# Performance work log

Hardware: AMD Instinct MI355X
Metric: run time of the kernel (lower is better)

Reference implementation:

```python
import jax, jax.numpy as jnp
import numpy as np

NUM_NODES = 100000
OUT_CHANNELS = 32
NUM_EDGES = 3200000


def setup_inputs() -> dict:
    key = jax.random.key(0)
    k1, k2, k3 = jax.random.split(key, 3)
    edge_index = jax.random.randint(k1, (2, NUM_EDGES), 0, NUM_NODES, dtype=jnp.int64)
    # nn.Linear init: weight [out, in], uniform(-1/sqrt(in), 1/sqrt(in))
    bound = 1.0 / np.sqrt(NUM_NODES)
    W = jax.random.uniform(k2, (OUT_CHANNELS, NUM_NODES), jnp.float32, -bound, bound)
    b = jax.random.uniform(k3, (OUT_CHANNELS,), jnp.float32, -bound, bound)
    return {"edge_index": edge_index, "W": W, "b": b}


def reference(edge_index, W, b):
    # LINK forward: A = sparse COO [N, num_nodes] with 1.0 per edge (duplicates sum),
    # logits = A @ W.T + b. Implemented as gather + segment_sum (no dense A).
    row = edge_index[0]
    col = edge_index[1]
    row = row - row.min()  # faithful to `row = row - row.min()`
    gathered = jnp.take(W.T, col, axis=0)  # [E, out_channels]
    logits = jax.ops.segment_sum(gathered, row, num_segments=NUM_NODES)  # [N, out]
    return logits + b
```

## Files before the change

kernel.cpp:

```cpp
#include <hip/hip_runtime.h>

#define NUM_NODES 100000
#define OUT_CH 32
#define NUM_EDGES 3200000

#define RPB 128
#define NB 782
#define CAP2 5120
#define TPB_BIN 1024
#define TILE 12800
#define KPT 13
#define NTILE 250
#define TPB 512
#define TR_BLOCKS 3125
#define MIN_BLOCKS 256

static __device__ __forceinline__ unsigned short f32_to_bf16_rne(float f) {
    unsigned u = __float_as_uint(f);
    unsigned r = u + 0x7FFFu + ((u >> 16) & 1u);
    return (unsigned short)(r >> 16);
}
static __device__ __forceinline__ float bf16_to_f32(unsigned short h) {
    return __uint_as_float(((unsigned)h) << 16);
}

__global__ void __launch_bounds__(256)
fused_pre(const float* __restrict__ W, ushort4* __restrict__ Wt,
          const int4* __restrict__ row4, int* __restrict__ partmin,
          int* __restrict__ bcount) {
    int bk = blockIdx.x;
    int t  = threadIdx.x;
    if (bk < TR_BLOCKS) {
        __shared__ float tile[32][33];
        int tx = t & 31, ty = t >> 5;
        int colBase = bk * 32;
        #pragma unroll
        for (int k = 0; k < 4; k++) {
            int c = ty + 8 * k;
            tile[c][tx] = W[c * NUM_NODES + colBase + tx];
        }
        __syncthreads();
        int lc = t >> 3, q = t & 7;
        ushort4 o;
        o.x = f32_to_bf16_rne(tile[q * 4 + 0][lc]);
        o.y = f32_to_bf16_rne(tile[q * 4 + 1][lc]);
        o.z = f32_to_bf16_rne(tile[q * 4 + 2][lc]);
        o.w = f32_to_bf16_rne(tile[q * 4 + 3][lc]);
        Wt[(size_t)(colBase + lc) * 8 + q] = o;
    } else if (bk < TR_BLOCKS + MIN_BLOCKS) {
        int mb  = bk - TR_BLOCKS;
        int tid = mb * 256 + t;
        int m = 0x7fffffff;
        for (int i = tid; i < NUM_EDGES / 4; i += MIN_BLOCKS * 256) {
            int4 v = row4[i];
            m = min(m, min(min(v.x, v.y), min(v.z, v.w)));
        }
        #pragma unroll
        for (int off = 32; off > 0; off >>= 1) m = min(m, __shfl_down(m, off, 64));
        __shared__ int wm[4];
        if ((t & 63) == 0) wm[t >> 6] = m;
        __syncthreads();
        if (t == 0) partmin[mb] = min(min(wm[0], wm[1]), min(wm[2], wm[3]));
    } else {
        for (int i = t; i < NB; i += 256) bcount[i] = 0;
    }
}

__global__ void __launch_bounds__(TPB_BIN)
bin_stage(const int* __restrict__ edge, const int* __restrict__ partmin,
          int* __restrict__ bcount, unsigned int* __restrict__ bin) {
    __shared__ int cnt[NB];
    __shared__ int cur[NB];
    __shared__ int rminS;
    int t = threadIdx.x;
    if (t < 64) {
        int m = min(min(partmin[t], partmin[t + 64]),
                    min(partmin[t + 128], partmin[t + 192]));
        #pragma unroll
        for (int off = 32; off > 0; off >>= 1) m = min(m, __shfl_down(m, off, 64));
        if (t == 0) rminS = m;
    }
    for (int i = t; i < NB; i += TPB_BIN) cnt[i] = 0;
    __syncthreads();
    int rmin = rminS;
    int eb = blockIdx.x * TILE;

    unsigned int ent[KPT];
    int bb[KPT];
    #pragma unroll
    for (int k = 0; k < KPT; k++) {
        int o = k * TPB_BIN + t;
        bb[k] = -1;
        if (o < TILE) {
            int e = eb + o;
            int r = edge[e] - rmin;
            int c = edge[NUM_EDGES + e];
            int b = r >> 7;
            bb[k]  = b;
            ent[k] = ((unsigned int)(r & 127) << 17) | (unsigned int)c;
            atomicAdd(&cnt[b], 1);
        }
    }
    __syncthreads();

    for (int i = t; i < NB; i += TPB_BIN) cur[i] = cnt[i] ? atomicAdd(&bcount[i], cnt[i]) : 0;
    __syncthreads();

    #pragma unroll
    for (int k = 0; k < KPT; k++) {
        if (bb[k] >= 0) {
            int pos = atomicAdd(&cur[bb[k]], 1);
            if (pos < CAP2) bin[(size_t)bb[k] * CAP2 + pos] = ent[k];
        }
    }
}

__global__ void __launch_bounds__(TPB)
bucket_gather(const unsigned int* __restrict__ bin, const int* __restrict__ bcount,
              const ushort4* __restrict__ Wt, const float* __restrict__ b,
              float* __restrict__ out) {
    __shared__ int cnt2[RPB * 8];
    __shared__ int cur2[RPB * 8];
    __shared__ int rowstart[RPB];
    __shared__ int rowcnt[RPB];
    __shared__ int scn[RPB];
    __shared__ int lcol[CAP2];

    int t = threadIdx.x;
    int bk = blockIdx.x;
    int n = bcount[bk];
    if (n > CAP2) n = CAP2;
    const unsigned int* mybin = bin + (size_t)bk * CAP2;

    for (int i = t; i < RPB * 8; i += TPB) cnt2[i] = 0;
    __syncthreads();

    for (int i = t; i < n; i += TPB) {
        unsigned int p = mybin[i];
        int lr  = p >> 17;
        int seg = (p & 0x1FFFF) >> 14;
        atomicAdd(&cnt2[(lr << 3) | seg], 1);
    }
    __syncthreads();

    if (t < RPB) {
        int s = 0;
        #pragma unroll
        for (int k = 0; k < 8; k++) s += cnt2[(t << 3) | k];
        rowcnt[t] = s;
        scn[t] = s;
    }
    __syncthreads();
    for (int off = 1; off < RPB; off <<= 1) {
        int v = (t < RPB && t >= off) ? scn[t - off] : 0;
        __syncthreads();
        if (t < RPB) scn[t] += v;
        __syncthreads();
    }
    if (t < RPB) {
        int rs = scn[t] - rowcnt[t];
        rowstart[t] = rs;
        int run = rs;
        #pragma unroll
        for (int k = 0; k < 8; k++) { cur2[(t << 3) | k] = run; run += cnt2[(t << 3) | k]; }
    }
    __syncthreads();

    for (int i = t; i < n; i += TPB) {
        unsigned int p = mybin[i];
        int lr = p >> 17;
        int c  = p & 0x1FFFF;
        int pos = atomicAdd(&cur2[(lr << 3) | (c >> 14)], 1);
        lcol[pos] = c;
    }
    __syncthreads();

    int g   = t >> 3;
    int sub = t & 7;
    float4 bias = ((const float4*)b)[sub];
    int lrA = g, lrB = g + 64;
    int rowA = bk * RPB + lrA;
    int rowB = bk * RPB + lrB;
    int iA = rowstart[lrA], eA = iA + rowcnt[lrA];
    int iB = rowstart[lrB], eB = iB + rowcnt[lrB];
    bool vA = rowA < NUM_NODES;
    bool vB = rowB < NUM_NODES;
    if (!vA) { iA = eA = 0; }
    if (!vB) { iB = eB = 0; }
    float4 accA = bias, accB = bias;
    int nPair = min(eA - iA, eB - iB);
    for (int k = 0; k < nPair; k++) {
        ushort4 wA = Wt[(size_t)lcol[iA + k] * 8 + sub];
        ushort4 wB = Wt[(size_t)lcol[iB + k] * 8 + sub];
        accA.x += bf16_to_f32(wA.x); accA.y += bf16_to_f32(wA.y);
        accA.z += bf16_to_f32(wA.z); accA.w += bf16_to_f32(wA.w);
        accB.x += bf16_to_f32(wB.x); accB.y += bf16_to_f32(wB.y);
        accB.z += bf16_to_f32(wB.z); accB.w += bf16_to_f32(wB.w);
    }
    iA += nPair; iB += nPair;
    for (; iA < eA; iA++) {
        ushort4 w = Wt[(size_t)lcol[iA] * 8 + sub];
        accA.x += bf16_to_f32(w.x); accA.y += bf16_to_f32(w.y);
        accA.z += bf16_to_f32(w.z); accA.w += bf16_to_f32(w.w);
    }
    for (; iB < eB; iB++) {
        ushort4 w = Wt[(size_t)lcol[iB] * 8 + sub];
        accB.x += bf16_to_f32(w.x); accB.y += bf16_to_f32(w.y);
        accB.z += bf16_to_f32(w.z); accB.w += bf16_to_f32(w.w);
    }
    if (vA) ((float4*)out)[(size_t)rowA * 8 + sub] = accA;
    if (vB) ((float4*)out)[(size_t)rowB * 8 + sub] = accB;
}

extern "C" void kernel_launch(void* const* d_in, const int* in_sizes, int n_in,
                              void* d_out, int out_size, void* d_ws, size_t ws_size,
                              hipStream_t stream) {
    const int*   edge = (const int*)d_in[0];
    const float* W    = (const float*)d_in[1];
    const float* b    = (const float*)d_in[2];
    float* out = (float*)d_out;

    char* ws = (char*)d_ws;
    int*          partmin = (int*)ws;
    int*          bcount  = (int*)(ws + 1024);
    ushort4*      Wt      = (ushort4*)(ws + 8192);
    unsigned int* bin     = (unsigned int*)(ws + 6422528);

    fused_pre<<<TR_BLOCKS + MIN_BLOCKS + 1, 256, 0, stream>>>(W, Wt, (const int4*)edge, partmin, bcount);
    bin_stage<<<NTILE, TPB_BIN, 0, stream>>>(edge, partmin, bcount, bin);
    bucket_gather<<<NB, TPB, 0, stream>>>(bin, bcount, Wt, b, out);
}
```

Measured before the change: 152.2 us.

## Stage binned edges in shared memory to coalesce global bin writes

The binning kernel now scatters each tile's entries into a shared-memory buffer sorted by bucket, using a block-wide prefix scan over bucket counts. Each thread then finds its element's bucket by binary search and writes to global memory, so consecutive threads write consecutive addresses within a bucket instead of scattering randomly. This adds a scan, a second shared-memory pass, a per-element binary search and about 60KB of extra shared memory per block, which may reduce occupancy.

```diff
diff --git a/kernel.cpp b/kernel.cpp
--- a/kernel.cpp
+++ b/kernel.cpp
@@ -69,8 +69,10 @@
 __global__ void __launch_bounds__(TPB_BIN)
 bin_stage(const int* __restrict__ edge, const int* __restrict__ partmin,
           int* __restrict__ bcount, unsigned int* __restrict__ bin) {
-    __shared__ int cnt[NB];
-    __shared__ int cur[NB];
+    __shared__ unsigned int sent[TILE];
+    __shared__ int scnt[NB];
+    __shared__ int send[NB];
+    __shared__ int gfix[NB];
     __shared__ int rminS;
     int t = threadIdx.x;
     if (t < 64) {
@@ -80,7 +82,7 @@
         for (int off = 32; off > 0; off >>= 1) m = min(m, __shfl_down(m, off, 64));
         if (t == 0) rminS = m;
     }
-    for (int i = t; i < NB; i += TPB_BIN) cnt[i] = 0;
+    if (t < NB) scnt[t] = 0;
     __syncthreads();
     int rmin = rminS;
     int eb = blockIdx.x * TILE;
@@ -98,19 +100,49 @@
             int b = r >> 7;
             bb[k]  = b;
             ent[k] = ((unsigned int)(r & 127) << 17) | (unsigned int)c;
-            atomicAdd(&cnt[b], 1);
-        }
-    }
-    __syncthreads();
-
-    for (int i = t; i < NB; i += TPB_BIN) cur[i] = cnt[i] ? atomicAdd(&bcount[i], cnt[i]) : 0;
+            atomicAdd(&scnt[b], 1);
+        }
+    }
+    __syncthreads();
+
+    if (t < NB) send[t] = scnt[t];
+    __syncthreads();
+    for (int off = 1; off < NB; off <<= 1) {
+        int v = 0;
+        if (t < NB && t >= off) v = send[t - off];
+        __syncthreads();
+        if (t < NB) send[t] += v;
+        __syncthreads();
+    }
+    if (t < NB) {
+        int inc = send[t];
+        int c   = scnt[t];
+        int ex  = inc - c;
+        int gb  = c ? atomicAdd(&bcount[t], c) : 0;
+        gfix[t] = t * CAP2 + gb - ex;
+        send[t] = ex;
+    }
     __syncthreads();
 
     #pragma unroll
     for (int k = 0; k < KPT; k++) {
         if (bb[k] >= 0) {
-            int pos = atomicAdd(&cur[bb[k]], 1);
-            if (pos < CAP2) bin[(size_t)bb[k] * CAP2 + pos] = ent[k];
+            int pos = atomicAdd(&send[bb[k]], 1);
+            sent[pos] = ent[k];
+        }
+    }
+    __syncthreads();
+
+    for (int k = 0; k < KPT; k++) {
+        int i = k * TPB_BIN + t;
+        if (i < TILE) {
+            int lo = 0, hi = NB - 1;
+            while (lo < hi) {
+                int mid = (lo + hi) >> 1;
+                if (send[mid] > i) hi = mid; else lo = mid + 1;
+            }
+            int dest = gfix[lo] + i;
+            if (dest < (lo + 1) * CAP2) bin[dest] = sent[i];
         }
     }
 }
```

After: 151.2 us. Within noise of the previous version (-0.7%).

## Fuse row-min reduction into binning kernel and apply offset at output

Applied to the files above, without the earlier changes.

Folds the row-min reduction and the binning pass into the transpose kernel, so the pipeline runs as two kernels plus memsets instead of three kernels. Edges are binned on raw row indices with a global atomicMin for the minimum, and the row shift is applied only when writing the output. Buckets shrink to 64 rows with 256-thread blocks, and the gather loop is unrolled by two for more loads in flight. In exchange it adds two memset launches and a global atomic. Bucket capacity is halved, so skewed row distributions are more likely to overflow.

```diff
diff --git a/kernel.cpp b/kernel.cpp
--- a/kernel.cpp
+++ b/kernel.cpp
@@ -4,16 +4,15 @@
 #define OUT_CH 32
 #define NUM_EDGES 3200000
 
-#define RPB 128
-#define NB 782
-#define CAP2 5120
-#define TPB_BIN 1024
-#define TILE 12800
-#define KPT 13
-#define NTILE 250
-#define TPB 512
+#define RPB 64
+#define NB 1563
+#define NBG 1564
+#define CAP2 2560
 #define TR_BLOCKS 3125
-#define MIN_BLOCKS 256
+#define BIN_TILE 3072
+#define BIN_KPT 12
+#define BIN_BLOCKS 1042
+#define TPB 256
 
 static __device__ __forceinline__ unsigned short f32_to_bf16_rne(float f) {
     unsigned u = __float_as_uint(f);
@@ -25,9 +24,9 @@
 }
 
 __global__ void __launch_bounds__(256)
-fused_pre(const float* __restrict__ W, ushort4* __restrict__ Wt,
-          const int4* __restrict__ row4, int* __restrict__ partmin,
-          int* __restrict__ bcount) {
+fused_main(const float* __restrict__ W, ushort4* __restrict__ Wt,
+           const int* __restrict__ edge, int* __restrict__ rminG,
+           int* __restrict__ bcount, unsigned int* __restrict__ bin) {
     int bk = blockIdx.x;
     int t  = threadIdx.x;
     if (bk < TR_BLOCKS) {
@@ -47,76 +46,53 @@
         o.z = f32_to_bf16_rne(tile[q * 4 + 2][lc]);
         o.w = f32_to_bf16_rne(tile[q * 4 + 3][lc]);
         Wt[(size_t)(colBase + lc) * 8 + q] = o;
-    } else if (bk < TR_BLOCKS + MIN_BLOCKS) {
-        int mb  = bk - TR_BLOCKS;
-        int tid = mb * 256 + t;
-        int m = 0x7fffffff;
-        for (int i = tid; i < NUM_EDGES / 4; i += MIN_BLOCKS * 256) {
-            int4 v = row4[i];
-            m = min(m, min(min(v.x, v.y), min(v.z, v.w)));
+    } else {
+        int mb = bk - TR_BLOCKS;
+        __shared__ int cnt[NB];
+        __shared__ int cur[NB];
+        __shared__ int wm[4];
+        for (int i = t; i < NB; i += 256) cnt[i] = 0;
+        int base = mb * BIN_TILE;
+        int nval = NUM_EDGES - base; if (nval > BIN_TILE) nval = BIN_TILE;
+        unsigned int ent[BIN_KPT];
+        int bb[BIN_KPT];
+        int rm = 0x7fffffff;
+        __syncthreads();
+        #pragma unroll
+        for (int k = 0; k < BIN_KPT; k++) {
+            int o = k * 256 + t;
+            bb[k] = -1;
+            if (o < nval) {
+                int e = base + o;
+                int r = edge[e];
+                int c = edge[NUM_EDGES + e];
+                rm = min(rm, r);
+                int b = r >> 6;
+                bb[k]  = b;
+                ent[k] = ((unsigned int)(r & 63) << 17) | (unsigned int)c;
+                atomicAdd(&cnt[b], 1);
+            }
         }
         #pragma unroll
-        for (int off = 32; off > 0; off >>= 1) m = min(m, __shfl_down(m, off, 64));
-        __shared__ int wm[4];
-        if ((t & 63) == 0) wm[t >> 6] = m;
-        __syncthreads();
-        if (t == 0) partmin[mb] = min(min(wm[0], wm[1]), min(wm[2], wm[3]));
-    } else {
-        for (int i = t; i < NB; i += 256) bcount[i] = 0;
-    }
-}
-
-__global__ void __launch_bounds__(TPB_BIN)
-bin_stage(const int* __restrict__ edge, const int* __restrict__ partmin,
-          int* __restrict__ bcount, unsigned int* __restrict__ bin) {
-    __shared__ int cnt[NB];
-    __shared__ int cur[NB];
-    __shared__ int rminS;
-    int t = threadIdx.x;
-    if (t < 64) {
-        int m = min(min(partmin[t], partmin[t + 64]),
-                    min(partmin[t + 128], partmin[t + 192]));
-        #pragma unroll
-        for (int off = 32; off > 0; off >>= 1) m = min(m, __shfl_down(m, off, 64));
-        if (t == 0) rminS = m;
-    }
-    for (int i = t; i < NB; i += TPB_BIN) cnt[i] = 0;
-    __syncthreads();
-    int rmin = rminS;
-    int eb = blockIdx.x * TILE;
-
-    unsigned int ent[KPT];
-    int bb[KPT];
-    #pragma unroll
-    for (int k = 0; k < KPT; k++) {
-        int o = k * TPB_BIN + t;
-        bb[k] = -1;
-        if (o < TILE) {
-            int e = eb + o;
-            int r = edge[e] - rmin;
-            int c = edge[NUM_EDGES + e];
-            int b = r >> 7;
-            bb[k]  = b;
-            ent[k] = ((unsigned int)(r & 127) << 17) | (unsigned int)c;
-            atomicAdd(&cnt[b], 1);
-        }
-    }
-    __syncthreads();
-
-    for (int i = t; i < NB; i += TPB_BIN) cur[i] = cnt[i] ? atomicAdd(&bcount[i], cnt[i]) : 0;
-    __syncthreads();
-
-    #pragma unroll
-    for (int k = 0; k < KPT; k++) {
-        if (bb[k] >= 0) {
-            int pos = atomicAdd(&cur[bb[k]], 1);
-            if (pos < CAP2) bin[(size_t)bb[k] * CAP2 + pos] = ent[k];
+        for (int off = 32; off > 0; off >>= 1) rm = min(rm, __shfl_down(rm, off, 64));
+        if ((t & 63) == 0) wm[t >> 6] = rm;
+        __syncthreads();
+        if (t == 0) atomicMin(rminG, min(min(wm[0], wm[1]), min(wm[2], wm[3])));
+        for (int i = t; i < NB; i += 256) cur[i] = cnt[i] ? atomicAdd(&bcount[i], cnt[i]) : 0;
+        __syncthreads();
+        #pragma unroll
+        for (int k = 0; k < BIN_KPT; k++) {
+            if (bb[k] >= 0) {
+                int pos = atomicAdd(&cur[bb[k]], 1);
+                if (pos < CAP2) bin[(size_t)bb[k] * CAP2 + pos] = ent[k];
+            }
         }
     }
 }
 
 __global__ void __launch_bounds__(TPB)
 bucket_gather(const unsigned int* __restrict__ bin, const int* __restrict__ bcount,
+              const int* __restrict__ rminG,
               const ushort4* __restrict__ Wt, const float* __restrict__ b,
               float* __restrict__ out) {
     __shared__ int cnt2[RPB * 8];
@@ -125,10 +101,12 @@
     __shared__ int rowcnt[RPB];
     __shared__ int scn[RPB];
     __shared__ int lcol[CAP2];
+    __shared__ int rminS;
 
     int t = threadIdx.x;
     int bk = blockIdx.x;
-    int n = bcount[bk];
+    if (t == 0) rminS = rminG[0];
+    int n = (bk < NB) ? bcount[bk] : 0;
     if (n > CAP2) n = CAP2;
     const unsigned int* mybin = bin + (size_t)bk * CAP2;
 
@@ -178,18 +156,36 @@
     int g   = t >> 3;
     int sub = t & 7;
     float4 bias = ((const float4*)b)[sub];
-    int lrA = g, lrB = g + 64;
-    int rowA = bk * RPB + lrA;
-    int rowB = bk * RPB + lrB;
+    int rmin = rminS;
+    int lrA = g, lrB = g + 32;
+    int outA = bk * RPB + lrA - rmin;
+    int outB = bk * RPB + lrB - rmin;
+    bool vA = (unsigned)outA < NUM_NODES;
+    bool vB = (unsigned)outB < NUM_NODES;
     int iA = rowstart[lrA], eA = iA + rowcnt[lrA];
     int iB = rowstart[lrB], eB = iB + rowcnt[lrB];
-    bool vA = rowA < NUM_NODES;
-    bool vB = rowB < NUM_NODES;
     if (!vA) { iA = eA = 0; }
     if (!vB) { iB = eB = 0; }
     float4 accA = bias, accB = bias;
     int nPair = min(eA - iA, eB - iB);
-    for (int k = 0; k < nPair; k++) {
+    int k = 0;
+    for (; k + 2 <= nPair; k += 2) {
+        int cA0 = lcol[iA + k],     cB0 = lcol[iB + k];
+        int cA1 = lcol[iA + k + 1], cB1 = lcol[iB + k + 1];
+        ushort4 wA0 = Wt[(size_t)cA0 * 8 + sub];
+        ushort4 wB0 = Wt[(size_t)cB0 * 8 + sub];
+        ushort4 wA1 = Wt[(size_t)cA1 * 8 + sub];
+        ushort4 wB1 = Wt[(size_t)cB1 * 8 + sub];
+        accA.x += bf16_to_f32(wA0.x) + bf16_to_f32(wA1.x);
+        accA.y += bf16_to_f32(wA0.y) + bf16_to_f32(wA1.y);
+        accA.z += bf16_to_f32(wA0.z) + bf16_to_f32(wA1.z);
+        accA.w += bf16_to_f32(wA0.w) + bf16_to_f32(wA1.w);
+        accB.x += bf16_to_f32(wB0.x) + bf16_to_f32(wB1.x);
+        accB.y += bf16_to_f32(wB0.y) + bf16_to_f32(wB1.y);
+        accB.z += bf16_to_f32(wB0.z) + bf16_to_f32(wB1.z);
+        accB.w += bf16_to_f32(wB0.w) + bf16_to_f32(wB1.w);
+    }
+    for (; k < nPair; k++) {
         ushort4 wA = Wt[(size_t)lcol[iA + k] * 8 + sub];
         ushort4 wB = Wt[(size_t)lcol[iB + k] * 8 + sub];
         accA.x += bf16_to_f32(wA.x); accA.y += bf16_to_f32(wA.y);
@@ -208,8 +204,8 @@
         accB.x += bf16_to_f32(w.x); accB.y += bf16_to_f32(w.y);
         accB.z += bf16_to_f32(w.z); accB.w += bf16_to_f32(w.w);
     }
-    if (vA) ((float4*)out)[(size_t)rowA * 8 + sub] = accA;
-    if (vB) ((float4*)out)[(size_t)rowB * 8 + sub] = accB;
+    if (vA) ((float4*)out)[(size_t)outA * 8 + sub] = accA;
+    if (vB) ((float4*)out)[(size_t)outB * 8 + sub] = accB;
 }
 
 extern "C" void kernel_launch(void* const* d_in, const int* in_sizes, int n_in,
@@ -221,12 +217,13 @@
     float* out = (float*)d_out;
 
     char* ws = (char*)d_ws;
-    int*          partmin = (int*)ws;
-    int*          bcount  = (int*)(ws + 1024);
-    ushort4*      Wt      = (ushort4*)(ws + 8192);
-    unsigned int* bin     = (unsigned int*)(ws + 6422528);
-
-    fused_pre<<<TR_BLOCKS + MIN_BLOCKS + 1, 256, 0, stream>>>(W, Wt, (const int4*)edge, partmin, bcount);
-    bin_stage<<<NTILE, TPB_BIN, 0, stream>>>(edge, partmin, bcount, bin);
-    bucket_gather<<<NB, TPB, 0, stream>>>(bin, bcount, Wt, b, out);
-}
+    int*          rminG  = (int*)ws;
+    int*          bcount = (int*)(ws + 1024);
+    ushort4*      Wt     = (ushort4*)(ws + 8192);
+    unsigned int* bin    = (unsigned int*)(ws + 6422528);
+
+    hipMemsetAsync(rminG, 0x7F, 4, stream);
+    hipMemsetAsync(bcount, 0, NBG * sizeof(int), stream);
+    fused_main<<<TR_BLOCKS + BIN_BLOCKS, 256, 0, stream>>>(W, Wt, edge, rminG, bcount, bin);
+    bucket_gather<<<NBG, TPB, 0, stream>>>(bin, bcount, rminG, Wt, b, out);
+}
```

After: 180.6 us. 18.6% more time.

## Fuse row-min into binning and merge transpose with bin stage

Applied to the files above, without the earlier changes.

Edges are now binned by raw row index, and the row minimum is computed in the same pass. Each bucket-gather block reduces the per-tile minima and applies the shift when it writes output rows. This drops the separate min-reduction pass over the row array and merges the W transpose and edge binning into one kernel launch, with 128-column transpose tiles and 1024 threads. Clearing bcount moves to a memset. When the row minimum is nonzero, the top output rows are never written, so they lose their bias-only values.

```diff
diff --git a/kernel.cpp b/kernel.cpp
--- a/kernel.cpp
+++ b/kernel.cpp
@@ -6,14 +6,14 @@
 
 #define RPB 128
 #define NB 782
+#define NBG 783
 #define CAP2 5120
-#define TPB_BIN 1024
+#define FTPB 1024
+#define TRB 782
+#define BINB 250
 #define TILE 12800
 #define KPT 13
-#define NTILE 250
 #define TPB 512
-#define TR_BLOCKS 3125
-#define MIN_BLOCKS 256
 
 static __device__ __forceinline__ unsigned short f32_to_bf16_rne(float f) {
     unsigned u = __float_as_uint(f);
@@ -24,99 +24,86 @@
     return __uint_as_float(((unsigned)h) << 16);
 }
 
-__global__ void __launch_bounds__(256)
+__global__ void __launch_bounds__(FTPB)
 fused_pre(const float* __restrict__ W, ushort4* __restrict__ Wt,
-          const int4* __restrict__ row4, int* __restrict__ partmin,
-          int* __restrict__ bcount) {
+          const int* __restrict__ edge, int* __restrict__ partmin,
+          int* __restrict__ bcount, unsigned int* __restrict__ bin) {
     int bk = blockIdx.x;
     int t  = threadIdx.x;
-    if (bk < TR_BLOCKS) {
-        __shared__ float tile[32][33];
-        int tx = t & 31, ty = t >> 5;
-        int colBase = bk * 32;
-        #pragma unroll
-        for (int k = 0; k < 4; k++) {
-            int c = ty + 8 * k;
-            tile[c][tx] = W[c * NUM_NODES + colBase + tx];
+    if (bk < TRB) {
+        __shared__ float tile[32][129];
+        int tx = t & 127, ty = t >> 7;
+        int colBase = bk * 128;
+        int col = colBase + tx;
+        if (col < NUM_NODES) {
+            #pragma unroll
+            for (int k = 0; k < 4; k++) {
+                int c = ty + 8 * k;
+                tile[c][tx] = W[(size_t)c * NUM_NODES + col];
+            }
         }
         __syncthreads();
         int lc = t >> 3, q = t & 7;
-        ushort4 o;
-        o.x = f32_to_bf16_rne(tile[q * 4 + 0][lc]);
-        o.y = f32_to_bf16_rne(tile[q * 4 + 1][lc]);
-        o.z = f32_to_bf16_rne(tile[q * 4 + 2][lc]);
-        o.w = f32_to_bf16_rne(tile[q * 4 + 3][lc]);
-        Wt[(size_t)(colBase + lc) * 8 + q] = o;
-    } else if (bk < TR_BLOCKS + MIN_BLOCKS) {
-        int mb  = bk - TR_BLOCKS;
-        int tid = mb * 256 + t;
-        int m = 0x7fffffff;
-        for (int i = tid; i < NUM_EDGES / 4; i += MIN_BLOCKS * 256) {
-            int4 v = row4[i];
-            m = min(m, min(min(v.x, v.y), min(v.z, v.w)));
-        }
-        #pragma unroll
-        for (int off = 32; off > 0; off >>= 1) m = min(m, __shfl_down(m, off, 64));
-        __shared__ int wm[4];
-        if ((t & 63) == 0) wm[t >> 6] = m;
-        __syncthreads();
-        if (t == 0) partmin[mb] = min(min(wm[0], wm[1]), min(wm[2], wm[3]));
+        int ocol = colBase + lc;
+        if (ocol < NUM_NODES) {
+            ushort4 o;
+            o.x = f32_to_bf16_rne(tile[q * 4 + 0][lc]);
+            o.y = f32_to_bf16_rne(tile[q * 4 + 1][lc]);
+            o.z = f32_to_bf16_rne(tile[q * 4 + 2][lc]);
+            o.w = f32_to_bf16_rne(tile[q * 4 + 3][lc]);
+            Wt[(size_t)ocol * 8 + q] = o;
+        }
     } else {
-        for (int i = t; i < NB; i += 256) bcount[i] = 0;
-    }
-}
-
-__global__ void __launch_bounds__(TPB_BIN)
-bin_stage(const int* __restrict__ edge, const int* __restrict__ partmin,
-          int* __restrict__ bcount, unsigned int* __restrict__ bin) {
-    __shared__ int cnt[NB];
-    __shared__ int cur[NB];
-    __shared__ int rminS;
-    int t = threadIdx.x;
-    if (t < 64) {
-        int m = min(min(partmin[t], partmin[t + 64]),
-                    min(partmin[t + 128], partmin[t + 192]));
-        #pragma unroll
-        for (int off = 32; off > 0; off >>= 1) m = min(m, __shfl_down(m, off, 64));
-        if (t == 0) rminS = m;
-    }
-    for (int i = t; i < NB; i += TPB_BIN) cnt[i] = 0;
-    __syncthreads();
-    int rmin = rminS;
-    int eb = blockIdx.x * TILE;
-
-    unsigned int ent[KPT];
-    int bb[KPT];
-    #pragma unroll
-    for (int k = 0; k < KPT; k++) {
-        int o = k * TPB_BIN + t;
-        bb[k] = -1;
-        if (o < TILE) {
-            int e = eb + o;
-            int r = edge[e] - rmin;
-            int c = edge[NUM_EDGES + e];
-            int b = r >> 7;
-            bb[k]  = b;
-            ent[k] = ((unsigned int)(r & 127) << 17) | (unsigned int)c;
-            atomicAdd(&cnt[b], 1);
-        }
-    }
-    __syncthreads();
-
-    for (int i = t; i < NB; i += TPB_BIN) cur[i] = cnt[i] ? atomicAdd(&bcount[i], cnt[i]) : 0;
-    __syncthreads();
-
-    #pragma unroll
-    for (int k = 0; k < KPT; k++) {
-        if (bb[k] >= 0) {
-            int pos = atomicAdd(&cur[bb[k]], 1);
-            if (pos < CAP2) bin[(size_t)bb[k] * CAP2 + pos] = ent[k];
+        int mb = bk - TRB;
+        __shared__ int cnt[NB];
+        __shared__ int cur[NB];
+        __shared__ int wm[16];
+        for (int i = t; i < NB; i += FTPB) cnt[i] = 0;
+        __syncthreads();
+        int base = mb * TILE;
+        unsigned int ent[KPT];
+        int bb[KPT];
+        int rm = 0x7fffffff;
+        #pragma unroll
+        for (int k = 0; k < KPT; k++) {
+            int o = k * FTPB + t;
+            bb[k] = -1;
+            if (o < TILE) {
+                int e = base + o;
+                int r = edge[e];
+                int c = edge[NUM_EDGES + e];
+                rm = min(rm, r);
+                int b = r >> 7;
+                bb[k]  = b;
+                ent[k] = ((unsigned int)(r & 127) << 17) | (unsigned int)c;
+                atomicAdd(&cnt[b], 1);
+            }
+        }
+        #pragma unroll
+        for (int off = 32; off > 0; off >>= 1) rm = min(rm, __shfl_down(rm, off, 64));
+        if ((t & 63) == 0) wm[t >> 6] = rm;
+        __syncthreads();
+        if (t == 0) {
+            int m = wm[0];
+            #pragma unroll
+            for (int w = 1; w < 16; w++) m = min(m, wm[w]);
+            partmin[mb] = m;
+        }
+        for (int i = t; i < NB; i += FTPB) cur[i] = cnt[i] ? atomicAdd(&bcount[i], cnt[i]) : 0;
+        __syncthreads();
+        #pragma unroll
+        for (int k = 0; k < KPT; k++) {
+            if (bb[k] >= 0) {
+                int pos = atomicAdd(&cur[bb[k]], 1);
+                if (pos < CAP2) bin[(size_t)bb[k] * CAP2 + pos] = ent[k];
+            }
         }
     }
 }
 
 __global__ void __launch_bounds__(TPB)
 bucket_gather(const unsigned int* __restrict__ bin, const int* __restrict__ bcount,
+              const int* __restrict__ partmin,
               const ushort4* __restrict__ Wt, const float* __restrict__ b,
               float* __restrict__ out) {
     __shared__ int cnt2[RPB * 8];
@@ -125,15 +112,28 @@
     __shared__ int rowcnt[RPB];
     __shared__ int scn[RPB];
     __shared__ int lcol[CAP2];
+    __shared__ int wmin[8];
+    __shared__ int rminS;
 
     int t = threadIdx.x;
     int bk = blockIdx.x;
-    int n = bcount[bk];
+    int pm = (t < BINB) ? partmin[t] : 0x7fffffff;
+    #pragma unroll
+    for (int off = 32; off > 0; off >>= 1) pm = min(pm, __shfl_down(pm, off, 64));
+    if ((t & 63) == 0) wmin[t >> 6] = pm;
+
+    int n = (bk < NB) ? bcount[bk] : 0;
     if (n > CAP2) n = CAP2;
     const unsigned int* mybin = bin + (size_t)bk * CAP2;
 
     for (int i = t; i < RPB * 8; i += TPB) cnt2[i] = 0;
     __syncthreads();
+    if (t == 0) {
+        int m = wmin[0];
+        #pragma unroll
+        for (int w = 1; w < 8; w++) m = min(m, wmin[w]);
+        rminS = m;
+    }
 
     for (int i = t; i < n; i += TPB) {
         unsigned int p = mybin[i];
@@ -178,13 +178,14 @@
     int g   = t >> 3;
     int sub = t & 7;
     float4 bias = ((const float4*)b)[sub];
+    int rmin = rminS;
     int lrA = g, lrB = g + 64;
-    int rowA = bk * RPB + lrA;
-    int rowB = bk * RPB + lrB;
+    int outA = bk * RPB + lrA - rmin;
+    int outB = bk * RPB + lrB - rmin;
+    bool vA = (unsigned)outA < NUM_NODES;
+    bool vB = (unsigned)outB < NUM_NODES;
     int iA = rowstart[lrA], eA = iA + rowcnt[lrA];
     int iB = rowstart[lrB], eB = iB + rowcnt[lrB];
-    bool vA = rowA < NUM_NODES;
-    bool vB = rowB < NUM_NODES;
     if (!vA) { iA = eA = 0; }
     if (!vB) { iB = eB = 0; }
     float4 accA = bias, accB = bias;
@@ -208,8 +209,8 @@
         accB.x += bf16_to_f32(w.x); accB.y += bf16_to_f32(w.y);
         accB.z += bf16_to_f32(w.z); accB.w += bf16_to_f32(w.w);
     }
-    if (vA) ((float4*)out)[(size_t)rowA * 8 + sub] = accA;
-    if (vB) ((float4*)out)[(size_t)rowB * 8 + sub] = accB;
+    if (vA) ((float4*)out)[(size_t)outA * 8 + sub] = accA;
+    if (vB) ((float4*)out)[(size_t)outB * 8 + sub] = accB;
 }
 
 extern "C" void kernel_launch(void* const* d_in, const int* in_sizes, int n_in,
@@ -226,7 +227,7 @@
     ushort4*      Wt      = (ushort4*)(ws + 8192);
     unsigned int* bin     = (unsigned int*)(ws + 6422528);
 
-    fused_pre<<<TR_BLOCKS + MIN_BLOCKS + 1, 256, 0, stream>>>(W, Wt, (const int4*)edge, partmin, bcount);
-    bin_stage<<<NTILE, TPB_BIN, 0, stream>>>(edge, partmin, bcount, bin);
-    bucket_gather<<<NB, TPB, 0, stream>>>(bin, bcount, Wt, b, out);
-}
+    hipMemsetAsync(bcount, 0, NBG * sizeof(int), stream);
+    fused_pre<<<TRB + BINB, FTPB, 0, stream>>>(W, Wt, edge, partmin, bcount, bin);
+    bucket_gather<<<NBG, TPB, 0, stream>>>(bin, bcount, partmin, Wt, b, out);
+}
```

Result: no change. 151.9 us (-0.2%).
